# Performance work log

Measured on AMD Instinct MI355X. Metric: run time of the kernel, lower is better.

Reference implementation:

```python
import jax, jax.numpy as jnp
import numpy as np

B, H, W, D = 16, 32, 32, 256
K = 8192


def setup_inputs() -> dict:
    key = jax.random.key(0)
    k1, k2 = jax.random.split(key)
    z_e = jax.random.normal(k1, (B, H, W, D), dtype=jnp.float32)
    # flax nn.initializers.uniform(scale=1.0) -> U[0, 1)
    codebook = jax.random.uniform(k2, (K, D), dtype=jnp.float32)
    return {"z_e": z_e, "codebook": codebook}


def reference(z_e, codebook):
    b, h, w, d = z_e.shape
    z_flat = z_e.reshape(-1, d)  # (N, D)
    # squared-euclidean distances: ||z||^2 + ||e||^2 - 2 z.e  -> (N, K)
    z2 = jnp.sum(z_flat ** 2, axis=1, keepdims=True)
    e2 = jnp.sum(codebook ** 2, axis=1)[None, :]
    dist = z2 + e2 - 2.0 * (z_flat @ codebook.T)
    idx = jnp.argmin(dist, axis=1)  # (N,)
    z_q = codebook[idx].reshape(b, h, w, d)
    # straight-through estimator
    z_st = z_e + jax.lax.stop_gradient(z_q - z_e)
    commit = jnp.mean((jax.lax.stop_gradient(z_q) - z_e) ** 2)
    codebook_loss = jnp.mean((z_q - jax.lax.stop_gradient(z_e)) ** 2)
    return z_st, idx.reshape(b, h, w), commit, codebook_loss
```

## Files before the change

### kernel.cpp

```cpp
#include <hip/hip_runtime.h>

#define NROWS 16384
#define KCODES 8192
#define DDIM 256
#define MARGIN 2.0f
#define SEG 192
#define NCT 16
#define GATHER_BLOCKS (NROWS / 16)

typedef __attribute__((ext_vector_type(8))) short short8;
typedef __attribute__((ext_vector_type(4))) float f32x4;

__device__ inline unsigned short f2bf(float x) {
    unsigned u = __float_as_uint(x);
    return (unsigned short)((u + 0x7FFFu + ((u >> 16) & 1u)) >> 16);
}

__device__ inline void gload16(const void* g, void* l) {
    __builtin_amdgcn_global_load_lds(
        (const __attribute__((address_space(1))) unsigned char*)g,
        (__attribute__((address_space(3))) unsigned char*)l, 16, 0, 0);
}

__device__ inline unsigned mbcnt64(unsigned long long m) {
    unsigned lo = __builtin_amdgcn_mbcnt_lo((unsigned)m, 0u);
    return __builtin_amdgcn_mbcnt_hi((unsigned)(m >> 32), lo);
}

__device__ inline void exact_rescore(const float* __restrict__ z, const float* __restrict__ cb,
                                     const float* __restrict__ z2g, const float* __restrict__ e2g,
                                     int grow, int gcol, unsigned long long* best) {
    const float4* av = reinterpret_cast<const float4*>(z + (size_t)grow * DDIM);
    const float4* bv = reinterpret_cast<const float4*>(cb + (size_t)gcol * DDIM);
    float dot = 0.f;
    #pragma unroll 8
    for (int j = 0; j < 64; ++j) {
        const float4 xa = av[j], xb = bv[j];
        dot = fmaf(xa.x, xb.x, fmaf(xa.y, xb.y, fmaf(xa.z, xb.z, fmaf(xa.w, xb.w, dot))));
    }
    const float de = z2g[grow] + e2g[gcol] - 2.0f * dot;
    const unsigned long long key =
        ((unsigned long long)__float_as_uint(de) << 32) | (unsigned)gcol;
    atomicMin(best + grow, key);
}

__global__ __launch_bounds__(256) void k_convert(
    const float* __restrict__ z, unsigned short* __restrict__ z_t,
    const float* __restrict__ cb, unsigned short* __restrict__ cb_t,
    float* __restrict__ z2, float* __restrict__ e2,
    unsigned long long* best, float* accum, unsigned* counters, unsigned* gctr)
{
    const int tid = threadIdx.x;
    const int bx = blockIdx.x;
    if (bx < 64) {
        const int gid = bx * 256 + tid;
        best[gid] = 0xFFFFFFFFFFFFFFFFull;
    }
    if (bx == 0) {
        if (tid < 16) counters[tid * 16] = 0u;
        if (tid == 0) { accum[0] = 0.0f; gctr[0] = 0u; }
    }
    const float* in;
    unsigned short* outt;
    float* sumsq;
    int g;
    if (bx < 256) { in = z;  outt = z_t;  sumsq = z2; g = bx * 4 + (tid >> 6); }
    else          { in = cb; outt = cb_t; sumsq = e2; g = (bx - 256) * 4 + (tid >> 6); }
    const int lane = tid & 63;
    const int row = g * 16 + (lane & 15);
    const int ko = (lane >> 4) * 8;
    float ss = 0.f;
    #pragma unroll
    for (int kb2 = 0; kb2 < 8; ++kb2) {
        const float4* src = reinterpret_cast<const float4*>(in + (size_t)row * DDIM + kb2 * 32 + ko);
        const float4 a = src[0], b = src[1];
        ss += a.x * a.x + a.y * a.y + a.z * a.z + a.w * a.w
            + b.x * b.x + b.y * b.y + b.z * b.z + b.w * b.w;
        short8 p;
        p[0] = (short)f2bf(a.x); p[1] = (short)f2bf(a.y); p[2] = (short)f2bf(a.z); p[3] = (short)f2bf(a.w);
        p[4] = (short)f2bf(b.x); p[5] = (short)f2bf(b.y); p[6] = (short)f2bf(b.z); p[7] = (short)f2bf(b.w);
        *reinterpret_cast<short8*>(outt + (((size_t)(g * 8 + kb2)) << 9) + lane * 8) = p;
    }
    ss += __shfl_xor(ss, 16);
    ss += __shfl_xor(ss, 32);
    if (lane < 16) sumsq[g * 16 + lane] = ss;
}

__global__ __launch_bounds__(1024, 4) void k_screen(
    const float* __restrict__ z, const float* __restrict__ cbp,
    const unsigned short* __restrict__ z_t, const unsigned short* __restrict__ cb_t,
    const float* __restrict__ z2g, const float* __restrict__ e2g,
    unsigned long long* __restrict__ best,
    unsigned* __restrict__ counters, unsigned* __restrict__ list, unsigned C16)
{
    __shared__ __align__(16) char smem[145664];
    char* ldsA = smem;
    char* ldsB = smem + 32768;
    float* rowmin = (float*)(smem + 131072);
    float* thrbuf = (float*)(smem + 133120);
    unsigned* wl_all = (unsigned*)(smem + 133376);

    const int tid = threadIdx.x;
    const int lane = tid & 63;
    const int wave = tid >> 6;
    const int wm = wave & 1;
    const int wn = wave >> 1;
    const int lhi = lane >> 4;
    const int llo = lane & 15;

    const int rt = blockIdx.x;
    const int row0 = rt * 64;

    #pragma unroll
    for (int i = 0; i < 2; ++i) {
        const int c = wave * 2 + i;
        gload16((const char*)z_t + (((size_t)((rt * 4 + (c >> 3)) * 8 + (c & 7))) << 10) + lane * 16,
                ldsA + c * 1024);
    }
    auto STAGE_B = [&](int b, int ct_, int kb2_) {
        #pragma unroll
        for (int i = 0; i < 2; ++i) {
            const int c = wave * 2 + i;
            gload16((const char*)cb_t + (((size_t)((ct_ * 32 + c) * 8 + kb2_)) << 10) + lane * 16,
                    ldsB + b * 32768 + c * 1024);
        }
    };
    STAGE_B(0, 0, 0);
    STAGE_B(1, 0, 1);
    if (tid < 64) thrbuf[tid] = 3.0e38f;
    __syncthreads();

    unsigned* wl = wl_all + wave * SEG;
    int S3 = 0;

    #pragma unroll 1
    for (int ci = 0; ci < NCT; ++ci) {
        f32x4 acc[2][4];
        #pragma unroll
        for (int i = 0; i < 2; ++i)
            #pragma unroll
            for (int j = 0; j < 4; ++j) { acc[i][j][0]=0.f; acc[i][j][1]=0.f; acc[i][j][2]=0.f; acc[i][j][3]=0.f; }

        #pragma unroll
        for (int kb2 = 0; kb2 < 8; ++kb2) {
            const int Sg = ci * 8 + kb2;
            int tb = S3 + 2; if (tb >= 3) tb -= 3;
            const int nS = Sg + 2;
            if (nS < NCT * 8) STAGE_B(tb, nS >> 3, nS & 7);

            char* bufB = ldsB + S3 * 32768;
            short8 bfr[4];
            #pragma unroll
            for (int fn = 0; fn < 4; ++fn)
                bfr[fn] = *reinterpret_cast<const short8*>(bufB + (wn * 4 + fn) * 1024 + lane * 16);
            #pragma unroll
            for (int fm = 0; fm < 2; ++fm) {
                const short8 af = *reinterpret_cast<const short8*>(
                    ldsA + (((wm * 2 + fm) * 8) + kb2) * 1024 + lane * 16);
                #pragma unroll
                for (int fn = 0; fn < 4; ++fn)
                    acc[fm][fn] = __builtin_amdgcn_mfma_f32_16x16x32_bf16(af, bfr[fn], acc[fm][fn], 0, 0, 0);
            }

            if (Sg >= NCT * 8 - 2) asm volatile("s_waitcnt vmcnt(0) lgkmcnt(0)" ::: "memory");
            else                   asm volatile("s_waitcnt vmcnt(2) lgkmcnt(0)" ::: "memory");
            __builtin_amdgcn_s_barrier();
            __builtin_amdgcn_sched_barrier(0);

            S3 = (S3 == 2) ? 0 : S3 + 1;
        }

        const int c0 = ci * 512 + wn * 64 + llo;
        float e2c[4];
        #pragma unroll
        for (int fn = 0; fn < 4; ++fn) e2c[fn] = e2g[c0 + fn * 16];

        #pragma unroll
        for (int fm = 0; fm < 2; ++fm) {
            #pragma unroll
            for (int rg = 0; rg < 4; ++rg) {
                const int rl = wm * 32 + fm * 16 + lhi * 4 + rg;
                float d[4];
                #pragma unroll
                for (int fn = 0; fn < 4; ++fn) d[fn] = fmaf(-2.0f, acc[fm][fn][rg], e2c[fn]);
                float m = fminf(fminf(d[0], d[1]), fminf(d[2], d[3]));
                #pragma unroll
                for (int off = 1; off < 16; off <<= 1) m = fminf(m, __shfl_xor(m, off));
                if (llo == 0) rowmin[wn * 64 + rl] = m;
            }
        }
        asm volatile("s_waitcnt lgkmcnt(0)" ::: "memory");
        __builtin_amdgcn_s_barrier();
        __builtin_amdgcn_sched_barrier(0);

        if (tid < 64) {
            float a = rowmin[tid];
            #pragma unroll
            for (int q = 1; q < 8; ++q) a = fminf(a, rowmin[q * 64 + tid]);
            thrbuf[tid] = fminf(thrbuf[tid], a);
        }
        asm volatile("s_waitcnt lgkmcnt(0)" ::: "memory");
        __builtin_amdgcn_s_barrier();
        __builtin_amdgcn_sched_barrier(0);

        unsigned wcount = 0;
        #pragma unroll
        for (int fm = 0; fm < 2; ++fm) {
            #pragma unroll
            for (int rg = 0; rg < 4; ++rg) {
                const int rl = wm * 32 + fm * 16 + lhi * 4 + rg;
                const float thr = thrbuf[rl] + MARGIN;
                float d[4];
                #pragma unroll
                for (int fn = 0; fn < 4; ++fn) d[fn] = fmaf(-2.0f, acc[fm][fn][rg], e2c[fn]);
                const bool hit = (d[0] <= thr) | (d[1] <= thr) | (d[2] <= thr) | (d[3] <= thr);
                if (__any(hit)) {
                    const int grow = row0 + rl;
                    #pragma unroll
                    for (int fn = 0; fn < 4; ++fn) {
                        const bool p = d[fn] <= thr;
                        const unsigned long long mask = __ballot(p);
                        if (mask) {
                            if (p) {
                                const unsigned pos = wcount + mbcnt64(mask);
                                const unsigned v = ((unsigned)grow << 13) | (unsigned)(c0 + fn * 16);
                                if (pos < SEG) wl[pos] = v;
                                else exact_rescore(z, cbp, z2g, e2g, grow, c0 + fn * 16, best);
                            }
                            wcount += (unsigned)__popcll(mask);
                        }
                    }
                }
            }
        }

        const unsigned n = wcount < SEG ? wcount : SEG;
        unsigned base = 0;
        if (lane == 0 && n) base = atomicAdd(&counters[wave * 16], n);
        base = (unsigned)__shfl((int)base, 0);
        for (unsigned i = lane; i < n; i += 64) {
            const unsigned v = wl[i];
            const unsigned slot = base + i;
            if (slot < C16) list[(size_t)wave * C16 + slot] = v;
            else exact_rescore(z, cbp, z2g, e2g, (int)(v >> 13), (int)(v & 8191u), best);
        }
    }
}

__global__ __launch_bounds__(256) void k_rescore(
    const float* __restrict__ z, const float* __restrict__ cbp,
    const float* __restrict__ z2g, const float* __restrict__ e2g,
    const unsigned* __restrict__ list, const unsigned* __restrict__ counters, unsigned C16,
    unsigned long long* best)
{
    const unsigned wid = (blockIdx.x * blockDim.x + threadIdx.x) >> 6;
    const unsigned nw = (gridDim.x * blockDim.x) >> 6;
    const int lane = threadIdx.x & 63;
    #pragma unroll 1
    for (int s = 0; s < 16; ++s) {
        const unsigned n = min(counters[s * 16], C16);
        const unsigned* shard = list + (size_t)s * C16;
        for (unsigned i = wid; i < n; i += nw) {
            const unsigned v = shard[i];
            const unsigned row = v >> 13, col = v & 8191u;
            const float4 a = *reinterpret_cast<const float4*>(z + (size_t)row * DDIM + lane * 4);
            const float4 b = *reinterpret_cast<const float4*>(cbp + (size_t)col * DDIM + lane * 4);
            float sdot = fmaf(a.x, b.x, fmaf(a.y, b.y, fmaf(a.z, b.z, a.w * b.w)));
            #pragma unroll
            for (int off = 1; off < 64; off <<= 1) sdot += __shfl_xor(sdot, off);
            if (lane == 0) {
                const float de = z2g[row] + e2g[col] - 2.0f * sdot;
                const unsigned long long key =
                    ((unsigned long long)__float_as_uint(de) << 32) | col;
                atomicMin(&best[row], key);
            }
        }
    }
}

__global__ __launch_bounds__(1024) void k_gather(
    const float* __restrict__ z, const float* __restrict__ cbp,
    const unsigned long long* __restrict__ best,
    float* __restrict__ out, float* __restrict__ accum, unsigned* __restrict__ gctr)
{
    __shared__ float wsum[16];
    const int tid = threadIdx.x;
    const int row = blockIdx.x * 16 + (tid >> 6);
    const int lane = tid & 63;
    const unsigned k = (unsigned)(best[row] & 0xFFFFFFFFull);
    const float4 ze = *reinterpret_cast<const float4*>(z + (size_t)row * DDIM + lane * 4);
    const float4 cq = *reinterpret_cast<const float4*>(cbp + (size_t)k * DDIM + lane * 4);
    float4 zst;
    zst.x = ze.x + (cq.x - ze.x); zst.y = ze.y + (cq.y - ze.y);
    zst.z = ze.z + (cq.z - ze.z); zst.w = ze.w + (cq.w - ze.w);
    *reinterpret_cast<float4*>(out + (size_t)row * DDIM + lane * 4) = zst;
    const float dx = cq.x - ze.x, dy = cq.y - ze.y, dz = cq.z - ze.z, dw = cq.w - ze.w;
    float s = dx * dx + dy * dy + dz * dz + dw * dw;
    #pragma unroll
    for (int off = 32; off > 0; off >>= 1) s += __shfl_down(s, off);
    if (lane == 0) {
        wsum[tid >> 6] = s;
        out[(size_t)NROWS * DDIM + row] = (float)k;
    }
    __syncthreads();
    if (tid == 0) {
        float tot = 0.f;
        #pragma unroll
        for (int i = 0; i < 16; ++i) tot += wsum[i];
        atomicAdd(accum, tot);
        __threadfence();
        const unsigned t = atomicAdd(gctr, 1u);
        if (t == GATHER_BLOCKS - 1) {
            const float total = atomicAdd(accum, 0.0f);
            const float m = total / (float)(NROWS * DDIM);
            out[(size_t)NROWS * DDIM + NROWS + 0] = m;
            out[(size_t)NROWS * DDIM + NROWS + 1] = m;
        }
    }
}

extern "C" void kernel_launch(void* const* d_in, const int* in_sizes, int n_in,
                              void* d_out, int out_size, void* d_ws, size_t ws_size,
                              hipStream_t stream)
{
    const float* z  = (const float*)d_in[0];
    const float* cb = (const float*)d_in[1];
    float* out = (float*)d_out;

    unsigned short* z_t  = (unsigned short*)d_out;
    unsigned short* cb_t = (unsigned short*)((char*)d_out + 8388608);

    char* ws = (char*)d_ws;
    unsigned long long* best = (unsigned long long*)ws;
    float* e2      = (float*)(ws + 131072);
    float* z2      = (float*)(ws + 163840);
    float* accum   = (float*)(ws + 229376);
    unsigned* gctr = (unsigned*)(ws + 229380);
    unsigned* counters = (unsigned*)(ws + 229440);
    unsigned* list = (unsigned*)(ws + 230464);
    unsigned C16 = 0;
    if (ws_size > 230464 + 64) {
        size_t c = (ws_size - 230464) / 4 / 16;
        if (c > (1u << 19)) c = (1u << 19);
        C16 = (unsigned)c;
    }

    k_convert<<<384, 256, 0, stream>>>(z, z_t, cb, cb_t, z2, e2, best, accum, counters, gctr);
    k_screen<<<256, 1024, 0, stream>>>(z, cb, z_t, cb_t, z2, e2, best, counters, list, C16);
    k_rescore<<<1024, 256, 0, stream>>>(z, cb, z2, e2, list, counters, C16, best);
    k_gather<<<GATHER_BLOCKS, 1024, 0, stream>>>(z, cb, best, out, accum, gctr);
}
```

Before: 214.7 us.

## Fuse z bf16 conversion and norms into screen kernel, halve screening margin

The z-side bf16 conversion and squared-norm computation move out of the convert kernel into the screen kernel prologue, which now writes bf16 z tiles straight into LDS instead of round-tripping a converted z buffer through global memory. The convert kernel now handles only the codebook with fewer blocks. The screening margin also drops from 2.0 to 1.0, so fewer candidates are sent to exact rescoring, at the risk of missing the true argmin when bf16 error exceeds the margin.

```diff
diff --git a/kernel.cpp b/kernel.cpp
--- a/kernel.cpp
+++ b/kernel.cpp
@@ -3,7 +3,7 @@
 #define NROWS 16384
 #define KCODES 8192
 #define DDIM 256
-#define MARGIN 2.0f
+#define MARGIN 1.0f
 #define SEG 192
 #define NCT 16
 #define GATHER_BLOCKS (NROWS / 16)
@@ -45,9 +45,8 @@
 }
 
 __global__ __launch_bounds__(256) void k_convert(
-    const float* __restrict__ z, unsigned short* __restrict__ z_t,
     const float* __restrict__ cb, unsigned short* __restrict__ cb_t,
-    float* __restrict__ z2, float* __restrict__ e2,
+    float* __restrict__ e2,
     unsigned long long* best, float* accum, unsigned* counters, unsigned* gctr)
 {
     const int tid = threadIdx.x;
@@ -60,36 +59,31 @@
         if (tid < 16) counters[tid * 16] = 0u;
         if (tid == 0) { accum[0] = 0.0f; gctr[0] = 0u; }
     }
-    const float* in;
-    unsigned short* outt;
-    float* sumsq;
-    int g;
-    if (bx < 256) { in = z;  outt = z_t;  sumsq = z2; g = bx * 4 + (tid >> 6); }
-    else          { in = cb; outt = cb_t; sumsq = e2; g = (bx - 256) * 4 + (tid >> 6); }
+    const int g = bx * 4 + (tid >> 6);
     const int lane = tid & 63;
     const int row = g * 16 + (lane & 15);
     const int ko = (lane >> 4) * 8;
     float ss = 0.f;
     #pragma unroll
     for (int kb2 = 0; kb2 < 8; ++kb2) {
-        const float4* src = reinterpret_cast<const float4*>(in + (size_t)row * DDIM + kb2 * 32 + ko);
+        const float4* src = reinterpret_cast<const float4*>(cb + (size_t)row * DDIM + kb2 * 32 + ko);
         const float4 a = src[0], b = src[1];
         ss += a.x * a.x + a.y * a.y + a.z * a.z + a.w * a.w
             + b.x * b.x + b.y * b.y + b.z * b.z + b.w * b.w;
         short8 p;
         p[0] = (short)f2bf(a.x); p[1] = (short)f2bf(a.y); p[2] = (short)f2bf(a.z); p[3] = (short)f2bf(a.w);
         p[4] = (short)f2bf(b.x); p[5] = (short)f2bf(b.y); p[6] = (short)f2bf(b.z); p[7] = (short)f2bf(b.w);
-        *reinterpret_cast<short8*>(outt + (((size_t)(g * 8 + kb2)) << 9) + lane * 8) = p;
+        *reinterpret_cast<short8*>(cb_t + (((size_t)(g * 8 + kb2)) << 9) + lane * 8) = p;
     }
     ss += __shfl_xor(ss, 16);
     ss += __shfl_xor(ss, 32);
-    if (lane < 16) sumsq[g * 16 + lane] = ss;
+    if (lane < 16) e2[g * 16 + lane] = ss;
 }
 
 __global__ __launch_bounds__(1024, 4) void k_screen(
     const float* __restrict__ z, const float* __restrict__ cbp,
-    const unsigned short* __restrict__ z_t, const unsigned short* __restrict__ cb_t,
-    const float* __restrict__ z2g, const float* __restrict__ e2g,
+    const unsigned short* __restrict__ cb_t,
+    float* z2g, const float* __restrict__ e2g,
     unsigned long long* __restrict__ best,
     unsigned* __restrict__ counters, unsigned* __restrict__ list, unsigned C16)
 {
@@ -111,12 +105,6 @@
     const int rt = blockIdx.x;
     const int row0 = rt * 64;
 
-    #pragma unroll
-    for (int i = 0; i < 2; ++i) {
-        const int c = wave * 2 + i;
-        gload16((const char*)z_t + (((size_t)((rt * 4 + (c >> 3)) * 8 + (c & 7))) << 10) + lane * 16,
-                ldsA + c * 1024);
-    }
     auto STAGE_B = [&](int b, int ct_, int kb2_) {
         #pragma unroll
         for (int i = 0; i < 2; ++i) {
@@ -127,6 +115,35 @@
     };
     STAGE_B(0, 0, 0);
     STAGE_B(1, 0, 1);
+
+    {
+        const int c = tid >> 5;
+        const int gl = c >> 3, kb2 = c & 7;
+        const int sp = (tid & 31) * 2;
+        #pragma unroll
+        for (int i = 0; i < 2; ++i) {
+            const int s = sp + i;
+            const int row = gl * 16 + (s & 15);
+            const int k = kb2 * 32 + (s >> 4) * 8;
+            const float4* src = reinterpret_cast<const float4*>(z + (size_t)(row0 + row) * DDIM + k);
+            const float4 a = src[0], b = src[1];
+            short8 p;
+            p[0] = (short)f2bf(a.x); p[1] = (short)f2bf(a.y); p[2] = (short)f2bf(a.z); p[3] = (short)f2bf(a.w);
+            p[4] = (short)f2bf(b.x); p[5] = (short)f2bf(b.y); p[6] = (short)f2bf(b.z); p[7] = (short)f2bf(b.w);
+            *reinterpret_cast<short8*>(ldsA + c * 1024 + s * 16) = p;
+        }
+    }
+
+    #pragma unroll
+    for (int rr = 0; rr < 4; ++rr) {
+        const int row = wave * 4 + rr;
+        const float4 v = *reinterpret_cast<const float4*>(z + (size_t)(row0 + row) * DDIM + lane * 4);
+        float s = v.x * v.x + v.y * v.y + v.z * v.z + v.w * v.w;
+        #pragma unroll
+        for (int off = 1; off < 64; off <<= 1) s += __shfl_xor(s, off);
+        if (lane == 0) z2g[row0 + row] = s;
+    }
+
     if (tid < 64) thrbuf[tid] = 3.0e38f;
     __syncthreads();
 
@@ -327,8 +344,7 @@
     const float* cb = (const float*)d_in[1];
     float* out = (float*)d_out;
 
-    unsigned short* z_t  = (unsigned short*)d_out;
-    unsigned short* cb_t = (unsigned short*)((char*)d_out + 8388608);
+    unsigned short* cb_t = (unsigned short*)d_out;
 
     char* ws = (char*)d_ws;
     unsigned long long* best = (unsigned long long*)ws;
@@ -345,8 +361,8 @@
         C16 = (unsigned)c;
     }
 
-    k_convert<<<384, 256, 0, stream>>>(z, z_t, cb, cb_t, z2, e2, best, accum, counters, gctr);
-    k_screen<<<256, 1024, 0, stream>>>(z, cb, z_t, cb_t, z2, e2, best, counters, list, C16);
+    k_convert<<<128, 256, 0, stream>>>(cb, cb_t, e2, best, accum, counters, gctr);
+    k_screen<<<256, 1024, 0, stream>>>(z, cb, cb_t, z2, e2, best, counters, list, C16);
     k_rescore<<<1024, 256, 0, stream>>>(z, cb, z2, e2, list, counters, C16, best);
     k_gather<<<GATHER_BLOCKS, 1024, 0, stream>>>(z, cb, best, out, accum, gctr);
 }
```

Result: no change. 212.3 us (-1.1%).
